# Performance work log

Hardware: AMD Instinct MI355X
Metric: run time of the kernel (lower is better)

## Reference

```python
import jax, jax.numpy as jnp
import numpy as np

S, B, L = 64, 32, 64          # seq_len (messages), batch (convs), max tokens per message
V, D = 32000, 300             # vocab, embedding dim
H = 512                       # hidden_dim; per-direction message hidden = H//2
F = 16                        # num_game_features
Hh = H // 2


def lstm_dir(x, mask, Wih, Whh, b, reverse=False):
    """Masked (packed-equivalent) LSTM. x:(T,N,D), mask:(T,N) bool.
    Returns h:(T,N,H) with zeros at invalid steps (matches pad_packed_sequence)."""
    if reverse:
        x, mask = x[::-1], mask[::-1]
    N = x.shape[1]
    Hd = Whh.shape[1]
    xg = jnp.einsum('tnd,gd->tng', x, Wih) + b  # (T,N,4H) input gates precomputed

    def step(carry, inp):
        h, c = carry
        xg_t, m = inp
        g = xg_t + h @ Whh.T
        i, f, gg, o = jnp.split(g, 4, axis=-1)
        c_new = jax.nn.sigmoid(f) * c + jax.nn.sigmoid(i) * jnp.tanh(gg)
        h_new = jax.nn.sigmoid(o) * jnp.tanh(c_new)
        m = m[:, None]
        return (jnp.where(m, h_new, h), jnp.where(m, c_new, c)), jnp.where(m, h_new, 0.0)

    init = (jnp.zeros((N, Hd), x.dtype), jnp.zeros((N, Hd), x.dtype))
    _, hs = jax.lax.scan(step, init, (xg, mask))
    if reverse:
        hs = hs[::-1]
    return hs


def setup_inputs() -> dict:
    key = jax.random.key(0)
    ks = jax.random.split(key, 16)
    s = 1.0 / np.sqrt(Hh)
    sc = 1.0 / np.sqrt(H)
    inp = {
        'messages': jax.random.randint(ks[0], (S, B, L), 0, V),
        'game_features': jax.random.normal(ks[1], (S, B, F), jnp.float32),
        'conv_lengths': jax.random.randint(ks[2], (B,), 1, S + 1),
        'E': jax.random.normal(ks[3], (V, D), jnp.float32) * 0.1,  # frozen embedding
        # message bi-LSTM (forward dir)
        'Wih_f': jax.random.uniform(ks[4], (4 * Hh, D), jnp.float32, -s, s),
        'Whh_f': jax.random.uniform(ks[5], (4 * Hh, Hh), jnp.float32, -s, s),
        'b_f': jax.random.uniform(ks[6], (4 * Hh,), jnp.float32, -s, s),
        # message bi-LSTM (backward dir)
        'Wih_b': jax.random.uniform(ks[7], (4 * Hh, D), jnp.float32, -s, s),
        'Whh_b': jax.random.uniform(ks[8], (4 * Hh, Hh), jnp.float32, -s, s),
        'b_b': jax.random.uniform(ks[9], (4 * Hh,), jnp.float32, -s, s),
        # conversation LSTM
        'Wih_c': jax.random.uniform(ks[10], (4 * H, H), jnp.float32, -sc, sc),
        'Whh_c': jax.random.uniform(ks[11], (4 * H, H), jnp.float32, -sc, sc),
        'b_c': jax.random.uniform(ks[12], (4 * H,), jnp.float32, -sc, sc),
        # classifier
        'Wc': jax.random.uniform(ks[13], (H + F,), jnp.float32, -sc, sc),
        'bc': jax.random.uniform(ks[14], (), jnp.float32, -sc, sc),
    }
    return inp


def reference(messages, game_features, conv_lengths, E, Wih_f, Whh_f, b_f,
              Wih_b, Whh_b, b_b, Wih_c, Whh_c, b_c, Wc, bc):
    # ---- message level: all S*B messages in one batched bi-LSTM pass ----
    flat = messages.reshape(S * B, L)                       # (N, L)
    emb = E[flat]                                           # (N, L, D)
    msg_len = jnp.maximum((flat != 0).sum(1), 1)            # clamp(min=1)
    tmask = jnp.arange(L)[:, None] < msg_len[None, :]       # (L, N)
    x = emb.transpose(1, 0, 2)                              # (L, N, D) time-major
    h_fwd = lstm_dir(x, tmask, Wih_f, Whh_f, b_f, reverse=False)
    h_bwd = lstm_dir(x, tmask, Wih_b, Whh_b, b_b, reverse=True)
    h = jnp.concatenate([h_fwd, h_bwd], axis=-1)            # (L, N, H); zeros at pad
    enc = h.max(axis=0)                                     # maxpool incl. zero pads (torch semantics)
    enc = enc.reshape(S, B, H)
    # ---- conversation level ----
    cmask = jnp.arange(S)[:, None] < conv_lengths[None, :]  # (S, B)
    conv_out = lstm_dir(enc, cmask, Wih_c, Whh_c, b_c)      # (S, B, H), zeros past length
    # dropout is identity at inference
    combined = jnp.concatenate([conv_out, game_features], axis=2)  # (S, B, H+F)
    logits = combined @ Wc + bc                             # (S, B)
    return logits
```

## Files before the change

kernel.cpp:

```cpp
#include <hip/hip_runtime.h>
#include <cmath>

#define S_DIM 64
#define B_DIM 32
#define L_DIM 64
#define NMSG  2048
#define D_DIM 300
#define HH    256
#define HC    512
#define F_DIM 16
#define VOCAB 32000

#define OFF_XGV   0u
#define OFF_WHH   32768000u
#define OFF_WPI   33030144u
#define OFF_WCI   33357824u
#define OFF_WCR   33882112u
#define OFF_ENCB  34406400u
#define OFF_HCONV 34930688u
#define OFF_CCONV 34938880u
#define OFF_CO    34955264u
#define OFF_MLEN  36003840u

typedef __attribute__((ext_vector_type(8))) short s8v;
typedef __attribute__((ext_vector_type(4))) float f4v;
#define MFMA(a,b,c) __builtin_amdgcn_mfma_f32_16x16x32_bf16((a),(b),(c),0,0,0)

__device__ __forceinline__ unsigned short f2bf(float x) {
    unsigned u = __float_as_uint(x);
    return (unsigned short)((u + 0x7FFFu + ((u >> 16) & 1u)) >> 16);
}
__device__ __forceinline__ float bf2f(unsigned short u) {
    return __uint_as_float(((unsigned)u) << 16);
}
__device__ __forceinline__ float sigm(float x) { return 1.0f / (1.0f + __expf(-x)); }
__device__ __forceinline__ float tanh_f(float x) { return 1.0f - 2.0f / (1.0f + __expf(2.0f * x)); }

__device__ __forceinline__ void gload16(const unsigned short* g, unsigned short* l) {
    __builtin_amdgcn_global_load_lds(
        (const __attribute__((address_space(1))) unsigned int*)g,
        (__attribute__((address_space(3))) unsigned int*)l, 16, 0, 0);
}

__global__ __launch_bounds__(256) void pack_whh(
    const float* __restrict__ Whh_f, const float* __restrict__ Whh_b,
    unsigned short* __restrict__ Wp)
{
    int nt = blockIdx.x, dir = blockIdx.y;
    const float* W = dir ? Whh_b : Whh_f;
    int tid = threadIdx.x, lane = tid & 63, ktq = tid >> 6;
    int n = nt * 16 + (lane & 15);
    int kb = (lane >> 4) * 8;
    #pragma unroll
    for (int pass = 0; pass < 2; ++pass) {
        int kt = ktq + pass * 4;
        int k0 = kt * 32 + kb;
        unsigned short tmp[8];
        #pragma unroll
        for (int u = 0; u < 8; ++u) tmp[u] = f2bf(W[(size_t)n * HH + k0 + u]);
        *(uint4*)(Wp + (size_t)dir * 262144 + ((size_t)(nt * 8 + kt)) * 512 + lane * 8) = *(uint4*)tmp;
    }
}

__global__ __launch_bounds__(256) void pack_wih(
    const float* __restrict__ Wih_f, const float* __restrict__ Wih_b,
    unsigned short* __restrict__ wpi)
{
    int nt = blockIdx.x, dir = blockIdx.y;
    const float* W = dir ? Wih_b : Wih_f;
    int tid = threadIdx.x, lane = tid & 63, ktq = tid >> 6;
    int n = nt * 16 + (lane & 15);
    int kb = (lane >> 4) * 8;
    for (int kt = ktq; kt < 10; kt += 4) {
        int k0 = kt * 32 + kb;
        unsigned short tmp[8];
        #pragma unroll
        for (int u = 0; u < 8; ++u) {
            int k = k0 + u;
            tmp[u] = (k < D_DIM) ? f2bf(W[(size_t)n * D_DIM + k]) : (unsigned short)0;
        }
        *(uint4*)(wpi + (size_t)dir * 327680 + ((size_t)(nt * 10 + kt)) * 512 + lane * 8) = *(uint4*)tmp;
    }
}

__global__ __launch_bounds__(256) void pack_whc(
    const float* __restrict__ Wih_c, const float* __restrict__ Whh_c,
    unsigned short* __restrict__ whci, unsigned short* __restrict__ whcr)
{
    int nt = blockIdx.x, which = blockIdx.y;
    const float* W = which ? Whh_c : Wih_c;
    unsigned short* dst = which ? whcr : whci;
    int tid = threadIdx.x, lane = tid & 63;
    int row = nt * 16 + (lane & 15);
    int kb = (lane >> 4) * 8;
    for (int kt = tid >> 6; kt < 16; kt += 4) {
        int k0 = kt * 32 + kb;
        unsigned short tmp[8];
        #pragma unroll
        for (int u = 0; u < 8; ++u) tmp[u] = f2bf(W[(size_t)row * HC + k0 + u]);
        *(uint4*)(dst + ((size_t)(nt * 16 + kt)) * 512 + lane * 8) = *(uint4*)tmp;
    }
}

__global__ __launch_bounds__(256) void msg_len_kernel(const int* __restrict__ msgs,
                                                      int* __restrict__ mlen) {
    int n = blockIdx.x * 256 + threadIdx.x;
    if (n >= NMSG) return;
    int cnt = 0;
    #pragma unroll 8
    for (int l = 0; l < L_DIM; ++l) cnt += (msgs[n * L_DIM + l] != 0);
    mlen[n] = max(cnt, 1);
}

__global__ __launch_bounds__(256) void init_conv(float* __restrict__ ws) {
    unsigned i = blockIdx.x * 256u + threadIdx.x;
    if (i < 24576u) ws[OFF_HCONV + i] = 0.0f;
}

#define EROW 328
__global__ __launch_bounds__(256) void xg_gemm(
    const float* __restrict__ E,
    const float* __restrict__ b_f, const float* __restrict__ b_b,
    const unsigned short* __restrict__ wpi,
    unsigned short* __restrict__ xgv)
{
    __shared__ __align__(16) unsigned short e_lds[32 * EROW];
    __shared__ __align__(16) float gbuf[32 * 264];
    const int w0 = blockIdx.x * 32;
    const int n0 = blockIdx.y * 256;
    const int dirb = n0 >> 10;
    const int nb = n0 & 1023;
    const float* bias = dirb ? b_b : b_f;

    const int tid = threadIdx.x, lane = tid & 63, wv = tid >> 6;
    const int l15 = lane & 15, kg = lane >> 4;

    for (int i = tid; i < 32 * 320; i += 256) {
        int r = i / 320, k = i - r * 320;
        float v = (k < D_DIM) ? E[(size_t)(w0 + r) * D_DIM + k] : 0.0f;
        e_lds[r * EROW + k] = f2bf(v);
    }
    __syncthreads();

    const unsigned short* wb = wpi + (size_t)dirb * 327680;
    const f4v zf = {0.0f, 0.0f, 0.0f, 0.0f};
    f4v acc[2][4];
    #pragma unroll
    for (int m = 0; m < 2; ++m)
        #pragma unroll
        for (int q = 0; q < 4; ++q) acc[m][q] = zf;

    for (int kt = 0; kt < 10; ++kt) {
        s8v a0 = *(const s8v*)&e_lds[l15 * EROW + kt * 32 + kg * 8];
        s8v a1 = *(const s8v*)&e_lds[(16 + l15) * EROW + kt * 32 + kg * 8];
        #pragma unroll
        for (int q = 0; q < 4; ++q) {
            int ntg = (nb >> 4) + wv * 4 + q;
            s8v b = *(const s8v*)(wb + ((size_t)(ntg * 10 + kt)) * 512 + lane * 8);
            acc[0][q] = MFMA(a0, b, acc[0][q]);
            acc[1][q] = MFMA(a1, b, acc[1][q]);
        }
    }

    #pragma unroll
    for (int q = 0; q < 4; ++q) {
        int col = (wv * 4 + q) * 16 + l15;
        float bv = bias[nb + col];
        #pragma unroll
        for (int m = 0; m < 2; ++m)
            #pragma unroll
            for (int r = 0; r < 4; ++r)
                gbuf[(m * 16 + kg * 4 + r) * 264 + col] = acc[m][q][r] + bv;
    }
    __syncthreads();
    {
        int row = tid >> 3, ch = tid & 7;
        unsigned short tmp[32];
        #pragma unroll
        for (int cc = 0; cc < 32; ++cc) tmp[cc] = f2bf(gbuf[row * 264 + ch * 32 + cc]);
        uint4* dst = (uint4*)(xgv + ((size_t)dirb * VOCAB + w0 + row) * 1024 + nb + ch * 32);
        const uint4* s4 = (const uint4*)tmp;
        #pragma unroll
        for (int u = 0; u < 4; ++u) dst[u] = s4[u];
    }
}

#define XGS  1032
#define HROW 264
__global__ __launch_bounds__(512, 2) void word_lstm(
    const int* __restrict__ msgs, const int* __restrict__ mlen,
    const unsigned short* __restrict__ xgv,
    const unsigned short* __restrict__ whh,
    unsigned short* __restrict__ enc_bf)
{
    __shared__ __align__(16) unsigned short xg_lds[2][16 * XGS];
    __shared__ __align__(16) unsigned short h_lds[16 * HROW];
    __shared__ int tok_s[16 * 64];
    __shared__ int len_s[16];

    const int mg = blockIdx.x >> 1, dir = blockIdx.x & 1;
    const int tid = threadIdx.x, lane = tid & 63, wv = tid >> 6;
    const int l15 = lane & 15, kg = lane >> 4;

    for (int i = tid; i < 16 * 64; i += 512) tok_s[i] = msgs[mg * 16 * 64 + i];
    if (tid < 16) len_s[tid] = mlen[mg * 16 + tid];
    for (int i = tid; i < 16 * HROW; i += 512) h_lds[i] = 0;
    __syncthreads();

    const unsigned short* xv = xgv + (size_t)dir * VOCAB * 1024;
    const unsigned short* wb = whh + (size_t)dir * 262144;

    int lens[4];
    #pragma unroll
    for (int r = 0; r < 4; ++r) lens[r] = len_s[kg * 4 + r];

    float c_st[2][4], rm[2][4];
    #pragma unroll
    for (int q = 0; q < 2; ++q)
        #pragma unroll
        for (int r = 0; r < 4; ++r) { c_st[q][r] = 0.0f; rm[q][r] = -INFINITY; }

    #pragma unroll
    for (int rr = 0; rr < 2; ++rr) {
        int row = wv * 2 + rr;
        int tt = dir ? (len_s[row] - 1) : 0;
        if (tt < 0) tt = 0;
        const unsigned short* src = xv + (size_t)tok_s[row * 64 + tt] * 1024 + lane * 8;
        gload16(src,       &xg_lds[0][row * XGS]);
        gload16(src + 512, &xg_lds[0][row * XGS + 512]);
    }

    for (int t = 0; t < L_DIM; ++t) {
        __syncthreads();
        const int buf = t & 1;

        f4v acc[2][4];
        #pragma unroll
        for (int q = 0; q < 2; ++q)
            #pragma unroll
            for (int g = 0; g < 4; ++g) {
                f4v v;
                #pragma unroll
                for (int r = 0; r < 4; ++r)
                    v[r] = bf2f(xg_lds[buf][(kg * 4 + r) * XGS + g * 256 + wv * 32 + q * 16 + l15]);
                acc[q][g] = v;
            }

        {
            s8v b0[8], b1[8];
            #pragma unroll
            for (int i = 0; i < 8; ++i)
                b0[i] = *(const s8v*)(wb + ((size_t)((((i >> 1) * 16 + wv * 2 + (i & 1)) * 8) + 0)) * 512 + lane * 8);
            #pragma unroll
            for (int kt = 0; kt < 8; kt += 2) {
                if (kt + 1 < 8) {
                    #pragma unroll
                    for (int i = 0; i < 8; ++i)
                        b1[i] = *(const s8v*)(wb + ((size_t)((((i >> 1) * 16 + wv * 2 + (i & 1)) * 8) + (kt + 1))) * 512 + lane * 8);
                }
                s8v a0 = *(const s8v*)&h_lds[l15 * HROW + kt * 32 + kg * 8];
                #pragma unroll
                for (int i = 0; i < 8; ++i)
                    acc[i & 1][i >> 1] = MFMA(a0, b0[i], acc[i & 1][i >> 1]);
                if (kt + 2 < 8) {
                    #pragma unroll
                    for (int i = 0; i < 8; ++i)
                        b0[i] = *(const s8v*)(wb + ((size_t)((((i >> 1) * 16 + wv * 2 + (i & 1)) * 8) + (kt + 2))) * 512 + lane * 8);
                }
                s8v a1 = *(const s8v*)&h_lds[l15 * HROW + (kt + 1) * 32 + kg * 8];
                #pragma unroll
                for (int i = 0; i < 8; ++i)
                    acc[i & 1][i >> 1] = MFMA(a1, b1[i], acc[i & 1][i >> 1]);
            }
        }

        if (t < 63) {
            #pragma unroll
            for (int rr = 0; rr < 2; ++rr) {
                int row = wv * 2 + rr;
                int tn = t + 1;
                int tt = dir ? (len_s[row] - 1 - tn) : tn;
                if (tt < 0) tt = 0;
                const unsigned short* src = xv + (size_t)tok_s[row * 64 + tt] * 1024 + lane * 8;
                gload16(src,       &xg_lds[buf ^ 1][row * XGS]);
                gload16(src + 512, &xg_lds[buf ^ 1][row * XGS + 512]);
            }
        }

        float hv[2][4];
        #pragma unroll
        for (int q = 0; q < 2; ++q)
            #pragma unroll
            for (int r = 0; r < 4; ++r) {
                float gi = acc[q][0][r], gf = acc[q][1][r], gc = acc[q][2][r], go = acc[q][3][r];
                float cn = sigm(gf) * c_st[q][r] + sigm(gi) * tanh_f(gc);
                float hn = sigm(go) * tanh_f(cn);
                hv[q][r] = hn;
                if (t < lens[r]) { c_st[q][r] = cn; rm[q][r] = fmaxf(rm[q][r], hn); }
                else             rm[q][r] = fmaxf(rm[q][r], 0.0f);
            }
        __syncthreads();
        #pragma unroll
        for (int q = 0; q < 2; ++q)
            #pragma unroll
            for (int r = 0; r < 4; ++r)
                if (t < lens[r])
                    h_lds[(kg * 4 + r) * HROW + wv * 32 + q * 16 + l15] = f2bf(hv[q][r]);
    }

    #pragma unroll
    for (int q = 0; q < 2; ++q)
        #pragma unroll
        for (int r = 0; r < 4; ++r)
            enc_bf[(size_t)(mg * 16 + kg * 4 + r) * HC + dir * HH + wv * 32 + q * 16 + l15] = f2bf(rm[q][r]);
}

#define CROW 520
__global__ __launch_bounds__(256) void xgc_gemm(
    const unsigned short* __restrict__ enc_bf,
    const unsigned short* __restrict__ whci,
    const float* __restrict__ b_c,
    unsigned short* __restrict__ xgc)
{
    __shared__ __align__(16) unsigned short e_lds[32 * CROW];
    const int m0 = blockIdx.x * 32;
    const int n0 = blockIdx.y * 256;
    const int tid = threadIdx.x, lane = tid & 63, wv = tid >> 6;
    const int l15 = lane & 15, kg = lane >> 4;

    for (int i = tid; i < 2048; i += 256) {
        int row = i >> 6, u4 = i & 63;
        ((uint4*)&e_lds[row * CROW])[u4] = ((const uint4*)(enc_bf + (size_t)(m0 + row) * HC))[u4];
    }
    __syncthreads();

    const f4v zf = {0.0f, 0.0f, 0.0f, 0.0f};
    f4v acc[2][4];
    #pragma unroll
    for (int m = 0; m < 2; ++m)
        #pragma unroll
        for (int q = 0; q < 4; ++q) acc[m][q] = zf;

    for (int kt = 0; kt < 16; ++kt) {
        s8v a0 = *(const s8v*)&e_lds[l15 * CROW + kt * 32 + kg * 8];
        s8v a1 = *(const s8v*)&e_lds[(16 + l15) * CROW + kt * 32 + kg * 8];
        #pragma unroll
        for (int q = 0; q < 4; ++q) {
            int nt = (n0 >> 4) + wv * 4 + q;
            s8v b = *(const s8v*)(whci + ((size_t)(nt * 16 + kt)) * 512 + lane * 8);
            acc[0][q] = MFMA(a0, b, acc[0][q]);
            acc[1][q] = MFMA(a1, b, acc[1][q]);
        }
    }

    #pragma unroll
    for (int q = 0; q < 4; ++q) {
        int col = n0 + (wv * 4 + q) * 16 + l15;
        float bv = b_c[col];
        #pragma unroll
        for (int m = 0; m < 2; ++m)
            #pragma unroll
            for (int r = 0; r < 4; ++r)
                xgc[(size_t)(m0 + m * 16 + kg * 4 + r) * 2048 + col] = f2bf(acc[m][q][r] + bv);
    }
}

__global__ __launch_bounds__(256) void conv_step(
    const unsigned short* __restrict__ whcr,
    const unsigned short* __restrict__ xgc,
    const int* __restrict__ conv_len,
    unsigned short* __restrict__ h_bf,
    float* __restrict__ c_ws,
    float* __restrict__ co,
    int s)
{
    __shared__ __align__(16) unsigned short xh[32 * CROW];
    __shared__ float gbuf[4][32][16];

    const int tid = threadIdx.x, jb = blockIdx.x;
    const int lane = tid & 63, g = tid >> 6;
    const int l15 = lane & 15, kg = lane >> 4;

    for (int i = tid; i < 2048; i += 256) {
        int row = i >> 6, u4 = i & 63;
        ((uint4*)&xh[row * CROW])[u4] = ((const uint4*)(h_bf + (size_t)row * HC))[u4];
    }
    __syncthreads();

    const int col = g * 512 + jb * 16 + l15;
    f4v acc0, acc1;
    #pragma unroll
    for (int r = 0; r < 4; ++r) {
        acc0[r] = bf2f(xgc[(size_t)(s * B_DIM + kg * 4 + r) * 2048 + col]);
        acc1[r] = bf2f(xgc[(size_t)(s * B_DIM + 16 + kg * 4 + r) * 2048 + col]);
    }

    const int nt = g * 32 + jb;
    for (int kt = 0; kt < 16; ++kt) {
        s8v a0 = *(const s8v*)&xh[l15 * CROW + kt * 32 + kg * 8];
        s8v a1 = *(const s8v*)&xh[(16 + l15) * CROW + kt * 32 + kg * 8];
        s8v b  = *(const s8v*)(whcr + ((size_t)(nt * 16 + kt)) * 512 + lane * 8);
        acc0 = MFMA(a0, b, acc0);
        acc1 = MFMA(a1, b, acc1);
    }

    #pragma unroll
    for (int r = 0; r < 4; ++r) {
        gbuf[g][kg * 4 + r][l15]      = acc0[r];
        gbuf[g][16 + kg * 4 + r][l15] = acc1[r];
    }
    __syncthreads();

    #pragma unroll
    for (int u = 0; u < 2; ++u) {
        int cell = tid + 256 * u;
        int b = cell >> 4, jj = cell & 15;
        int j = jb * 16 + jj;
        bool valid = s < conv_len[b];
        float g_i = gbuf[0][b][jj], g_f = gbuf[1][b][jj];
        float g_c = gbuf[2][b][jj], g_o = gbuf[3][b][jj];
        float cold = c_ws[b * HC + j];
        float cn = sigm(g_f) * cold + sigm(g_i) * tanh_f(g_c);
        float hn = sigm(g_o) * tanh_f(cn);
        float outv = 0.0f;
        if (valid) {
            c_ws[b * HC + j] = cn;
            h_bf[b * HC + j] = f2bf(hn);
            outv = hn;
        }
        co[((size_t)s * B_DIM + b) * HC + j] = outv;
    }
}

__global__ __launch_bounds__(256) void logits_kernel(
    const float* __restrict__ gfeat, const float* __restrict__ Wc, const float* __restrict__ bc,
    const float* __restrict__ co, float* __restrict__ out)
{
    int o = blockIdx.x * 4 + (threadIdx.x >> 6);
    int lane = threadIdx.x & 63;
    const float* row = co + (size_t)o * HC;
    float sum = 0.0f;
    #pragma unroll
    for (int u = 0; u < 8; ++u) sum += row[lane + 64 * u] * Wc[lane + 64 * u];
    if (lane < F_DIM) sum += gfeat[o * F_DIM + lane] * Wc[HC + lane];
    #pragma unroll
    for (int off = 32; off > 0; off >>= 1) sum += __shfl_down(sum, off, 64);
    if (lane == 0) out[o] = sum + bc[0];
}

extern "C" void kernel_launch(void* const* d_in, const int* in_sizes, int n_in,
                              void* d_out, int out_size, void* d_ws, size_t ws_size,
                              hipStream_t stream) {
    const int*   msgs    = (const int*)  d_in[0];
    const float* gfeat   = (const float*)d_in[1];
    const int*   convlen = (const int*)  d_in[2];
    const float* E       = (const float*)d_in[3];
    const float* Wih_f   = (const float*)d_in[4];
    const float* Whh_f   = (const float*)d_in[5];
    const float* b_f     = (const float*)d_in[6];
    const float* Wih_b   = (const float*)d_in[7];
    const float* Whh_b   = (const float*)d_in[8];
    const float* b_b     = (const float*)d_in[9];
    const float* Wih_c   = (const float*)d_in[10];
    const float* Whh_c   = (const float*)d_in[11];
    const float* b_c     = (const float*)d_in[12];
    const float* Wc      = (const float*)d_in[13];
    const float* bc      = (const float*)d_in[14];
    float* out = (float*)d_out;
    float* ws  = (float*)d_ws;

    unsigned short* xgv    = (unsigned short*)(ws + OFF_XGV);
    unsigned short* xgc    = (unsigned short*)(ws + OFF_XGV);
    unsigned short* whh    = (unsigned short*)(ws + OFF_WHH);
    unsigned short* wpi    = (unsigned short*)(ws + OFF_WPI);
    unsigned short* whci   = (unsigned short*)(ws + OFF_WCI);
    unsigned short* whcr   = (unsigned short*)(ws + OFF_WCR);
    unsigned short* enc_bf = (unsigned short*)(ws + OFF_ENCB);
    unsigned short* h_bf   = (unsigned short*)(ws + OFF_HCONV);
    float*          c_ws   = ws + OFF_CCONV;
    float*          co     = ws + OFF_CO;
    int*            mlen   = (int*)(ws + OFF_MLEN);

    pack_whh<<<dim3(64, 2), 256, 0, stream>>>(Whh_f, Whh_b, whh);
    pack_wih<<<dim3(64, 2), 256, 0, stream>>>(Wih_f, Wih_b, wpi);
    pack_whc<<<dim3(128, 2), 256, 0, stream>>>(Wih_c, Whh_c, whci, whcr);
    msg_len_kernel<<<NMSG / 256, 256, 0, stream>>>(msgs, mlen);
    init_conv<<<96, 256, 0, stream>>>(ws);
    xg_gemm<<<dim3(1000, 8), 256, 0, stream>>>(E, b_f, b_b, wpi, xgv);

    word_lstm<<<256, 512, 0, stream>>>(msgs, mlen, xgv, whh, enc_bf);

    xgc_gemm<<<dim3(64, 8), 256, 0, stream>>>(enc_bf, whci, b_c, xgc);

    for (int s = 0; s < S_DIM; ++s)
        conv_step<<<32, 256, 0, stream>>>(whcr, xgc, convlen, h_bf, c_ws, co, s);

    logits_kernel<<<NMSG / 4, 256, 0, stream>>>(gfeat, Wc, bc, co, out);
}
```

Measured before the change: 1.388 ms.

## Keep half of recurrent weights in registers and stop at group max length

Half of the word-LSTM recurrent weight fragments (gates i and f) are loaded once into registers before the time loop, and only the other half is reloaded from global memory each step. The time loop now runs only to the longest message in the 16-message group instead of all 64 steps. The zero-pad max is applied once at the end for messages shorter than 64. The next-step xg prefetch is issued before the MFMA work to overlap better. Holding 32 extra vector registers per thread may hurt occupancy under the (512,2) launch bound, and the saving from early stop depends on how message lengths are distributed.

```diff
diff --git a/kernel.cpp b/kernel.cpp
--- a/kernel.cpp
+++ b/kernel.cpp
@@ -202,7 +202,7 @@
     const int tid = threadIdx.x, lane = tid & 63, wv = tid >> 6;
     const int l15 = lane & 15, kg = lane >> 4;
 
-    for (int i = tid; i < 16 * 64; i += 512) tok_s[i] = msgs[mg * 16 * 64 + i];
+    for (int i = tid; i < 16 * 64; i += 512) tok_s[i] = msgs[mg * 1024 + i];
     if (tid < 16) len_s[tid] = mlen[mg * 16 + tid];
     for (int i = tid; i < 16 * HROW; i += 512) h_lds[i] = 0;
     __syncthreads();
@@ -210,9 +210,25 @@
     const unsigned short* xv = xgv + (size_t)dir * VOCAB * 1024;
     const unsigned short* wb = whh + (size_t)dir * 262144;
 
+    s8v bw[4][8];
+    #pragma unroll
+    for (int i = 0; i < 4; ++i)
+        #pragma unroll
+        for (int kt = 0; kt < 8; ++kt)
+            bw[i][kt] = *(const s8v*)(wb + ((size_t)((((i >> 1) * 16 + wv * 2 + (i & 1)) * 8) + kt)) * 512 + lane * 8);
+    #pragma unroll
+    for (int i = 0; i < 4; ++i)
+        #pragma unroll
+        for (int kt = 0; kt < 8; ++kt)
+            asm volatile("" : "+v"(bw[i][kt]));
+
     int lens[4];
     #pragma unroll
     for (int r = 0; r < 4; ++r) lens[r] = len_s[kg * 4 + r];
+
+    int bmax = 1;
+    #pragma unroll
+    for (int i = 0; i < 16; ++i) bmax = max(bmax, len_s[i]);
 
     float c_st[2][4], rm[2][4];
     #pragma unroll
@@ -230,51 +246,11 @@
         gload16(src + 512, &xg_lds[0][row * XGS + 512]);
     }
 
-    for (int t = 0; t < L_DIM; ++t) {
+    for (int t = 0; t < bmax; ++t) {
         __syncthreads();
         const int buf = t & 1;
 
-        f4v acc[2][4];
-        #pragma unroll
-        for (int q = 0; q < 2; ++q)
-            #pragma unroll
-            for (int g = 0; g < 4; ++g) {
-                f4v v;
-                #pragma unroll
-                for (int r = 0; r < 4; ++r)
-                    v[r] = bf2f(xg_lds[buf][(kg * 4 + r) * XGS + g * 256 + wv * 32 + q * 16 + l15]);
-                acc[q][g] = v;
-            }
-
-        {
-            s8v b0[8], b1[8];
-            #pragma unroll
-            for (int i = 0; i < 8; ++i)
-                b0[i] = *(const s8v*)(wb + ((size_t)((((i >> 1) * 16 + wv * 2 + (i & 1)) * 8) + 0)) * 512 + lane * 8);
-            #pragma unroll
-            for (int kt = 0; kt < 8; kt += 2) {
-                if (kt + 1 < 8) {
-                    #pragma unroll
-                    for (int i = 0; i < 8; ++i)
-                        b1[i] = *(const s8v*)(wb + ((size_t)((((i >> 1) * 16 + wv * 2 + (i & 1)) * 8) + (kt + 1))) * 512 + lane * 8);
-                }
-                s8v a0 = *(const s8v*)&h_lds[l15 * HROW + kt * 32 + kg * 8];
-                #pragma unroll
-                for (int i = 0; i < 8; ++i)
-                    acc[i & 1][i >> 1] = MFMA(a0, b0[i], acc[i & 1][i >> 1]);
-                if (kt + 2 < 8) {
-                    #pragma unroll
-                    for (int i = 0; i < 8; ++i)
-                        b0[i] = *(const s8v*)(wb + ((size_t)((((i >> 1) * 16 + wv * 2 + (i & 1)) * 8) + (kt + 2))) * 512 + lane * 8);
-                }
-                s8v a1 = *(const s8v*)&h_lds[l15 * HROW + (kt + 1) * 32 + kg * 8];
-                #pragma unroll
-                for (int i = 0; i < 8; ++i)
-                    acc[i & 1][i >> 1] = MFMA(a1, b1[i], acc[i & 1][i >> 1]);
-            }
-        }
-
-        if (t < 63) {
+        if (t + 1 < bmax) {
             #pragma unroll
             for (int rr = 0; rr < 2; ++rr) {
                 int row = wv * 2 + rr;
@@ -287,6 +263,31 @@
             }
         }
 
+        f4v acc[2][4];
+        #pragma unroll
+        for (int q = 0; q < 2; ++q)
+            #pragma unroll
+            for (int g = 0; g < 4; ++g) {
+                f4v v;
+                #pragma unroll
+                for (int r = 0; r < 4; ++r)
+                    v[r] = bf2f(xg_lds[buf][(kg * 4 + r) * XGS + g * 256 + wv * 32 + q * 16 + l15]);
+                acc[q][g] = v;
+            }
+
+        #pragma unroll
+        for (int kt = 0; kt < 8; ++kt) {
+            s8v a = *(const s8v*)&h_lds[l15 * HROW + kt * 32 + kg * 8];
+            #pragma unroll
+            for (int i = 0; i < 4; ++i)
+                acc[i & 1][i >> 1] = MFMA(a, bw[i][kt], acc[i & 1][i >> 1]);
+            #pragma unroll
+            for (int i = 4; i < 8; ++i) {
+                s8v b = *(const s8v*)(wb + ((size_t)((((i >> 1) * 16 + wv * 2 + (i & 1)) * 8) + kt)) * 512 + lane * 8);
+                acc[i & 1][i >> 1] = MFMA(a, b, acc[i & 1][i >> 1]);
+            }
+        }
+
         float hv[2][4];
         #pragma unroll
         for (int q = 0; q < 2; ++q)
@@ -297,7 +298,6 @@
                 float hn = sigm(go) * tanh_f(cn);
                 hv[q][r] = hn;
                 if (t < lens[r]) { c_st[q][r] = cn; rm[q][r] = fmaxf(rm[q][r], hn); }
-                else             rm[q][r] = fmaxf(rm[q][r], 0.0f);
             }
         __syncthreads();
         #pragma unroll
@@ -311,8 +311,11 @@
     #pragma unroll
     for (int q = 0; q < 2; ++q)
         #pragma unroll
-        for (int r = 0; r < 4; ++r)
-            enc_bf[(size_t)(mg * 16 + kg * 4 + r) * HC + dir * HH + wv * 32 + q * 16 + l15] = f2bf(rm[q][r]);
+        for (int r = 0; r < 4; ++r) {
+            float v = rm[q][r];
+            if (lens[r] < 64) v = fmaxf(v, 0.0f);
+            enc_bf[(size_t)(mg * 16 + kg * 4 + r) * HC + dir * HH + wv * 32 + q * 16 + l15] = f2bf(v);
+        }
 }
 
 #define CROW 520
```

Measured after the change: 1.333 ms. 1.04x faster.
